# Kernel tuning notes

Hardware: AMD Instinct MI355X
Metric: run time of the kernel (lower is better)

The kernel has to match this reference:

```python
import jax, jax.numpy as jnp
import numpy as np

B, T, C, H = 512, 1024, 64, 128


def setup_inputs() -> dict:
    key = jax.random.key(0)
    ks = jax.random.split(key, 7)
    s = 1.0 / np.sqrt(H)  # PyTorch LSTM/Linear default init U(-1/sqrt(H), 1/sqrt(H))
    u = lambda k, shape: jax.random.uniform(k, shape, jnp.float32, -s, s)
    return {
        "x": jax.random.normal(ks[0], (B, T, C), jnp.float32),
        # Per-channel stacked LSTM params; input_size=1 so W_ih is [C, 4H]
        "W_ih": u(ks[1], (C, 4 * H)),
        "W_hh": u(ks[2], (C, 4 * H, H)),
        "b_ih": u(ks[3], (C, 4 * H)),
        "b_hh": u(ks[4], (C, 4 * H)),
        # Per-channel final Linear(H, 1)
        "W_fc": u(ks[5], (C, H)),
        "b_fc": u(ks[6], (C,)),
    }


def reference(x, W_ih, W_hh, b_ih, b_hh, W_fc, b_fc):
    # x: [B, T, C]. All channels' LSTMs run as one fused vectorized scan.
    Bx, Tx, Cx = x.shape
    Hh = W_hh.shape[-1]
    b = b_ih + b_hh  # [C, 4H]
    xt = jnp.transpose(x, (1, 0, 2))  # [T, B, C]
    h0 = jnp.zeros((Bx, Cx, Hh), x.dtype)
    c0 = jnp.zeros((Bx, Cx, Hh), x.dtype)

    def step(carry, x_t):
        h, c = carry  # each [B, C, H]
        gates = (jnp.einsum('bc,cg->bcg', x_t, W_ih)
                 + jnp.einsum('bch,cgh->bcg', h, W_hh)
                 + b)  # [B, C, 4H]
        i, f, g, o = jnp.split(gates, 4, axis=-1)  # PyTorch gate order: i, f, g, o
        i = jax.nn.sigmoid(i)
        f = jax.nn.sigmoid(f)
        g = jnp.tanh(g)
        o = jax.nn.sigmoid(o)
        c = f * c + i * g
        h = o * jnp.tanh(c)
        return (h, c), None

    (h_last, _), _ = jax.lax.scan(step, (h0, c0), xt)
    # Per-channel Linear(H, 1) on the final hidden state, then squeeze -> [B, C]
    return jnp.einsum('bch,ch->bc', h_last, W_fc) + b_fc
```

## Files before the change

### kernel.cpp

```cpp
#include <hip/hip_runtime.h>


typedef _Float16 half8 __attribute__((ext_vector_type(8)));
typedef float floatx4 __attribute__((ext_vector_type(4)));

#define LOG2E 1.44269504088896340736f

__global__ __launch_bounds__(512, 2) void lstm_fused(
    const float* __restrict__ x,
    const float* __restrict__ Wih,
    const float* __restrict__ Whh,
    const float* __restrict__ bih,
    const float* __restrict__ bhh,
    const float* __restrict__ Wfc,
    const float* __restrict__ bfc,
    float* __restrict__ out)
{
    constexpr int T = 1024, C = 64, H = 128, G = 512;
    constexpr int TC = T * C;

    __shared__ _Float16 hbuf[8192];
    __shared__ float xstage[2][64];

    const int bid = blockIdx.x;
    const int ch  = bid & 63;
    const int b0  = (bid >> 6) << 6;

    const int tid = threadIdx.x;
    const int w   = tid >> 6;
    const int l   = tid & 63;
    const int q   = l >> 4;
    const int li  = l & 15;

    float wihr[4], bias[4];
    half8 Wf[4][4];
#pragma unroll
    for (int ct = 0; ct < 4; ++ct) {
        const float sc = (ct == 2) ? 2.0f * LOG2E : LOG2E;
        const int col = ct * H + w * 16 + li;
        wihr[ct] = Wih[ch * G + col] * sc;
        bias[ct] = (bih[ch * G + col] + bhh[ch * G + col]) * sc;
#pragma unroll
        for (int ks = 0; ks < 4; ++ks) {
            const float* wp = &Whh[((size_t)(ch * G + col)) * H + ks * 32 + q * 8];
            half8 hv;
#pragma unroll
            for (int j = 0; j < 8; ++j) hv[j] = (_Float16)(wp[j] * sc);
            Wf[ct][ks] = hv;
        }
    }

    for (int i = tid; i < 8192; i += 512) hbuf[i] = (_Float16)0.0f;

    const float* xrow = x + (size_t)(b0 + (tid & 63)) * TC + ch;
    if (tid < 64) xstage[0][tid] = xrow[0];

    float cst[4][4];
#pragma unroll
    for (int rt = 0; rt < 4; ++rt)
#pragma unroll
        for (int r = 0; r < 4; ++r) cst[rt][r] = 0.0f;

    const int ks_w = w >> 1;
    const int qq_w = ((w & 1) << 1) + (li >> 3);
    const int j_w  = li & 7;
    const int rxor = qq_w & 3;
    int wel[4];
#pragma unroll
    for (int r = 0; r < 4; ++r)
        wel[r] = ks_w * 512 + (qq_w * 16 + q * 4 + (r ^ rxor)) * 8 + j_w;
    const int rdoff = (q * 16 + (li ^ (q & 3))) * 8;

    __syncthreads();

    for (int t = 0; t < T; ++t) {
        const int tn = (t + 1 < T) ? t + 1 : T - 1;
        float xpre;
        if (tid < 64) xpre = xrow[tn * C];
        const float* xcur = xstage[t & 1];

        _Float16 hreg[16];

#pragma unroll
        for (int rt = 0; rt < 4; ++rt) {
            const floatx4 xq = *(const floatx4*)&xcur[rt * 16 + q * 4];

            floatx4 acc[4];
#pragma unroll
            for (int ct = 0; ct < 4; ++ct)
#pragma unroll
                for (int r = 0; r < 4; ++r)
                    acc[ct][r] = fmaf(xq[r], wihr[ct], bias[ct]);

#pragma unroll
            for (int ks = 0; ks < 4; ++ks) {
                const half8 a = *(const half8*)&hbuf[(rt * 4 + ks) * 512 + rdoff];
#pragma unroll
                for (int ct = 0; ct < 4; ++ct)
                    acc[ct] = __builtin_amdgcn_mfma_f32_16x16x32_f16(a, Wf[ct][ks], acc[ct], 0, 0, 0);
            }

#pragma unroll
            for (int r = 0; r < 4; ++r) {
                const float u  = __builtin_amdgcn_exp2f(-acc[0][r]);
                const float v  = __builtin_amdgcn_exp2f(-acc[1][r]);
                const float p  = __builtin_amdgcn_exp2f(acc[2][r]);
                const float wq = __builtin_amdgcn_exp2f(-acc[3][r]);
                const float Du = 1.0f + u, Dv = 1.0f + v;
                const float Dp = 1.0f + p, Dw = 1.0f + wq;
                const float A  = Du * Dv, Bq = Dp * Dw;
                const float R  = __builtin_amdgcn_rcpf(A * Bq);
                const float RA = R * Bq;
                const float RB = R * A;
                const float ig = Dv * RA;
                const float fg = Du * RA;
                const float tg = fmaf(-2.0f, Dw * RB, 1.0f);
                const float og = Dp * RB;
                const float cn = fmaf(fg, cst[rt][r], ig * tg);
                cst[rt][r] = cn;
                const float tq = __builtin_amdgcn_fmed3f(
                    cn * (2.0f * LOG2E), -29.0f, 29.0f);
                const float hq = fmaf(-2.0f,
                    __builtin_amdgcn_rcpf(1.0f + __builtin_amdgcn_exp2f(tq)), 1.0f);
                hreg[rt * 4 + r] = (_Float16)(og * hq);
            }
        }

        __syncthreads();

#pragma unroll
        for (int rt = 0; rt < 4; ++rt)
#pragma unroll
            for (int r = 0; r < 4; ++r)
                hbuf[rt * 2048 + wel[r]] = hreg[rt * 4 + r];
        if (tid < 64) xstage[(t + 1) & 1][tid] = xpre;

        __syncthreads();
    }

    if (tid < 64) {
        const int row = tid;
        const int rt = row >> 4, m = row & 15;
        float s = bfc[ch];
#pragma unroll
        for (int hh = 0; hh < H; ++hh) {
            const int ks = hh >> 5, qq = (hh & 31) >> 3, j = hh & 7;
            const int c = qq * 16 + (m ^ (qq & 3));
            s += (float)hbuf[(rt * 4 + ks) * 512 + c * 8 + j] * Wfc[ch * H + hh];
        }
        out[(size_t)(b0 + row) * C + ch] = s;
    }
}

extern "C" void kernel_launch(void* const* d_in, const int* in_sizes, int n_in,
                              void* d_out, int out_size, void* d_ws, size_t ws_size,
                              hipStream_t stream) {
    const float* x   = (const float*)d_in[0];
    const float* Wih = (const float*)d_in[1];
    const float* Whh = (const float*)d_in[2];
    const float* bih = (const float*)d_in[3];
    const float* bhh = (const float*)d_in[4];
    const float* Wfc = (const float*)d_in[5];
    const float* bfc = (const float*)d_in[6];
    float* out = (float*)d_out;

    lstm_fused<<<512, 512, 0, stream>>>(x, Wih, Whh, bih, bhh, Wfc, bfc, out);
}
```

Measured before the change: 6.186 ms.

## Software-pipeline LSTM step across row tiles to overlap MFMA with activations

Restructures the time step into a skewed pipeline: MFMA for row tile rt+1 is issued while activations for row tile rt run, using two accumulator sets and writing h straight into shared memory per tile instead of buffering it all until the end. Barriers are placed per tile phase, so the step goes from two syncs to four. The aim is to hide MFMA latency behind transcendental VALU work within a wave. Launch bounds are relaxed to one block per CU to free registers for the extra accumulators, which may reduce occupancy-based latency hiding.

After: 6.334 ms. 1.02x slower.

```diff
diff --git a/kernel.cpp b/kernel.cpp
--- a/kernel.cpp
+++ b/kernel.cpp
@@ -6,7 +6,7 @@
 
 #define LOG2E 1.44269504088896340736f
 
-__global__ __launch_bounds__(512, 2) void lstm_fused(
+__global__ __launch_bounds__(512, 1) void lstm_fused(
     const float* __restrict__ x,
     const float* __restrict__ Wih,
     const float* __restrict__ Whh,
@@ -20,7 +20,7 @@
     constexpr int TC = T * C;
 
     __shared__ _Float16 hbuf[8192];
-    __shared__ float xstage[2][64];
+    __shared__ float xs[2][64];
 
     const int bid = blockIdx.x;
     const int ch  = bid & 63;
@@ -53,7 +53,7 @@
     for (int i = tid; i < 8192; i += 512) hbuf[i] = (_Float16)0.0f;
 
     const float* xrow = x + (size_t)(b0 + (tid & 63)) * TC + ch;
-    if (tid < 64) xstage[0][tid] = xrow[0];
+    if (tid < 64) xs[0][tid] = xrow[0];
 
     float cst[4][4];
 #pragma unroll
@@ -71,72 +71,81 @@
         wel[r] = ks_w * 512 + (qq_w * 16 + q * 4 + (r ^ rxor)) * 8 + j_w;
     const int rdoff = (q * 16 + (li ^ (q & 3))) * 8;
 
+    floatx4 acc0[4], acc1[4];
+    float xpre = 0.0f;
+
+    auto mfma_phase = [&](int rt, const float* __restrict__ xcur,
+                          floatx4* __restrict__ acc) {
+        const floatx4 xq = *(const floatx4*)&xcur[rt * 16 + q * 4];
+#pragma unroll
+        for (int ct = 0; ct < 4; ++ct)
+#pragma unroll
+            for (int r = 0; r < 4; ++r)
+                acc[ct][r] = fmaf(xq[r], wihr[ct], bias[ct]);
+#pragma unroll
+        for (int ks = 0; ks < 4; ++ks) {
+            const half8 a = *(const half8*)&hbuf[(rt * 4 + ks) * 512 + rdoff];
+#pragma unroll
+            for (int ct = 0; ct < 4; ++ct)
+                acc[ct] = __builtin_amdgcn_mfma_f32_16x16x32_f16(a, Wf[ct][ks], acc[ct], 0, 0, 0);
+        }
+    };
+
+    auto act_phase = [&](int rt, const floatx4* __restrict__ acc) {
+#pragma unroll
+        for (int r = 0; r < 4; ++r) {
+            const float u  = __builtin_amdgcn_exp2f(-acc[0][r]);
+            const float v  = __builtin_amdgcn_exp2f(-acc[1][r]);
+            const float p  = __builtin_amdgcn_exp2f(acc[2][r]);
+            const float wq = __builtin_amdgcn_exp2f(-acc[3][r]);
+            const float Du = 1.0f + u, Dv = 1.0f + v;
+            const float Dp = 1.0f + p, Dw = 1.0f + wq;
+            const float A  = Du * Dv, Bq = Dp * Dw;
+            const float R  = __builtin_amdgcn_rcpf(A * Bq);
+            const float RA = R * Bq;
+            const float RB = R * A;
+            const float ig = Dv * RA;
+            const float fg = Du * RA;
+            const float tg = fmaf(-2.0f, Dw * RB, 1.0f);
+            const float og = Dp * RB;
+            const float cn = fmaf(fg, cst[rt][r], ig * tg);
+            cst[rt][r] = cn;
+            const float tq = __builtin_amdgcn_fmed3f(
+                cn * (2.0f * LOG2E), -29.0f, 29.0f);
+            const float hq = fmaf(-2.0f,
+                __builtin_amdgcn_rcpf(1.0f + __builtin_amdgcn_exp2f(tq)), 1.0f);
+            hbuf[rt * 2048 + wel[r]] = (_Float16)(og * hq);
+        }
+    };
+
+    __syncthreads();
+
+    mfma_phase(0, xs[0], acc0);
+    if (tid < 64) xpre = xrow[C];
     __syncthreads();
 
     for (int t = 0; t < T; ++t) {
-        const int tn = (t + 1 < T) ? t + 1 : T - 1;
-        float xpre;
-        if (tid < 64) xpre = xrow[tn * C];
-        const float* xcur = xstage[t & 1];
+        const float* xcur = xs[t & 1];
+        act_phase(0, acc0);
+        mfma_phase(1, xcur, acc1);
+        if (tid < 64) xs[(t + 1) & 1][tid] = xpre;
+        __syncthreads();
+        act_phase(1, acc1);
+        mfma_phase(2, xcur, acc0);
+        __syncthreads();
+        act_phase(2, acc0);
+        mfma_phase(3, xcur, acc1);
+        __syncthreads();
+        act_phase(3, acc1);
+        if (t + 1 < T) {
+            mfma_phase(0, xs[(t + 1) & 1], acc0);
+            const int tn = (t + 2 < T) ? t + 2 : T - 1;
+            if (tid < 64) xpre = xrow[tn * C];
+            __syncthreads();
+        }
+    }
 
-        _Float16 hreg[16];
-
-#pragma unroll
-        for (int rt = 0; rt < 4; ++rt) {
-            const floatx4 xq = *(const floatx4*)&xcur[rt * 16 + q * 4];
-
-            floatx4 acc[4];
-#pragma unroll
-            for (int ct = 0; ct < 4; ++ct)
-#pragma unroll
-                for (int r = 0; r < 4; ++r)
-                    acc[ct][r] = fmaf(xq[r], wihr[ct], bias[ct]);
-
-#pragma unroll
-            for (int ks = 0; ks < 4; ++ks) {
-                const half8 a = *(const half8*)&hbuf[(rt * 4 + ks) * 512 + rdoff];
-#pragma unroll
-                for (int ct = 0; ct < 4; ++ct)
-                    acc[ct] = __builtin_amdgcn_mfma_f32_16x16x32_f16(a, Wf[ct][ks], acc[ct], 0, 0, 0);
-            }
-
-#pragma unroll
-            for (int r = 0; r < 4; ++r) {
-                const float u  = __builtin_amdgcn_exp2f(-acc[0][r]);
-                const float v  = __builtin_amdgcn_exp2f(-acc[1][r]);
-                const float p  = __builtin_amdgcn_exp2f(acc[2][r]);
-                const float wq = __builtin_amdgcn_exp2f(-acc[3][r]);
-                const float Du = 1.0f + u, Dv = 1.0f + v;
-                const float Dp = 1.0f + p, Dw = 1.0f + wq;
-                const float A  = Du * Dv, Bq = Dp * Dw;
-                const float R  = __builtin_amdgcn_rcpf(A * Bq);
-                const float RA = R * Bq;
-                const float RB = R * A;
-                const float ig = Dv * RA;
-                const float fg = Du * RA;
-                const float tg = fmaf(-2.0f, Dw * RB, 1.0f);
-                const float og = Dp * RB;
-                const float cn = fmaf(fg, cst[rt][r], ig * tg);
-                cst[rt][r] = cn;
-                const float tq = __builtin_amdgcn_fmed3f(
-                    cn * (2.0f * LOG2E), -29.0f, 29.0f);
-                const float hq = fmaf(-2.0f,
-                    __builtin_amdgcn_rcpf(1.0f + __builtin_amdgcn_exp2f(tq)), 1.0f);
-                hreg[rt * 4 + r] = (_Float16)(og * hq);
-            }
-        }
-
-        __syncthreads();
-
-#pragma unroll
-        for (int rt = 0; rt < 4; ++rt)
-#pragma unroll
-            for (int r = 0; r < 4; ++r)
-                hbuf[rt * 2048 + wel[r]] = hreg[rt * 4 + r];
-        if (tid < 64) xstage[(t + 1) & 1][tid] = xpre;
-
-        __syncthreads();
-    }
+    __syncthreads();
 
     if (tid < 64) {
         const int row = tid;
```
